# Kernel optimization log

Measured on AMD Instinct MI355X. Metric: run time of the kernel, lower is better.

## Reference

```python
import jax, jax.numpy as jnp
import numpy as np

B, NS, NT = 8, 1024, 1024
SRC, TGT, OUT, H = 1024, 1024, 1024, 8
DH = OUT // H  # per-head dim = 128


def setup_inputs() -> dict:
    key = jax.random.key(0)
    ks = jax.random.split(key, 9)
    s = 0.02
    return {
        "src": jax.random.normal(ks[0], (B, NS, SRC), jnp.float32),
        "tgt": jax.random.normal(ks[1], (B, NT, TGT), jnp.float32),
        "src_mask": jnp.ones((B, NS), jnp.float32),
        "tgt_mask": jnp.ones((B, NT), jnp.float32),
        "Ws": jax.random.normal(ks[2], (2 * OUT, SRC), jnp.float32) * s,
        "bs": jnp.zeros((2 * OUT,), jnp.float32),
        "Wt": jax.random.normal(ks[3], (OUT, TGT), jnp.float32) * s,
        "bt": jnp.zeros((OUT,), jnp.float32),
        "Wo": jax.random.normal(ks[4], (OUT, OUT + TGT), jnp.float32) * s,
        "bo": jnp.zeros((OUT,), jnp.float32),
    }


def reference(src, tgt, src_mask, tgt_mask, Ws, bs, Wt, bt, Wo, bo):
    # src_lin / tgt_lin (FCNet = linear, no activation, drop=0 at eval)
    src_trans = jnp.einsum("bsf,of->bso", src, Ws) + bs  # [B,NS,2*OUT]
    tgt_trans = jnp.einsum("btf,of->bto", tgt, Wt) + bt  # [B,NT,OUT]
    src_trans = src_trans * src_mask[:, :, None]
    tgt_trans = tgt_trans * tgt_mask[:, :, None]

    src_key, src_val = jnp.split(src_trans, 2, axis=2)  # each [B,NS,OUT]
    # head split along channels == reshape to [.., H, DH]
    k = src_key.reshape(B, NS, H, DH)
    v = src_val.reshape(B, NS, H, DH)
    q = tgt_trans.reshape(B, NT, H, DH)

    scores = jnp.einsum("bthd,bshd->bhts", q, k) / jnp.sqrt(jnp.float32(DH))
    scores = jnp.where(src_mask[:, None, None, :] == 0, -jnp.inf, scores)
    attn = jax.nn.softmax(scores, axis=-1)  # [B,H,NT,NS]
    tgt_update = jnp.einsum("bhts,bshd->bthd", attn, v).reshape(B, NT, OUT)

    cat_tgt = jnp.concatenate([tgt, tgt_update], axis=2)  # [B,NT,TGT+OUT]
    update_tgt = jnp.einsum("btf,of->bto", cat_tgt, Wo) + bo
    return update_tgt
```

## Files before the change

### kernel.cpp

```cpp
#include <hip/hip_runtime.h>


typedef __bf16 bf16x8 __attribute__((ext_vector_type(8)));
typedef float f32x4 __attribute__((ext_vector_type(4)));
typedef unsigned short u16;
typedef unsigned short u16x8 __attribute__((ext_vector_type(8)));

#define MFMA16(a, b, c) __builtin_amdgcn_mfma_f32_16x16x32_bf16((a), (b), (c), 0, 0, 0)

__device__ __forceinline__ float bf2f(u16 b) {
  return __uint_as_float(((unsigned)b) << 16);
}
__device__ __forceinline__ u16 f2bf(float f) {
  unsigned u = __float_as_uint(f);
  u += 0x7fffu + ((u >> 16) & 1u);
  return (u16)(u >> 16);
}

__device__ __forceinline__ void async16(const u16* g, u16* l) {
  __builtin_amdgcn_global_load_lds(
      (const __attribute__((address_space(1))) unsigned int*)g,
      (__attribute__((address_space(3))) unsigned int*)l, 16, 0, 0);
}

struct Cvt5 {
  const float* src[5];
  unsigned cnt4[5];
  unsigned ooff[5];
};

__global__ __launch_bounds__(256)
void cvt5_kernel(Cvt5 a, u16* __restrict__ out, unsigned total4)
{
  unsigned gid = blockIdx.x * 256u + threadIdx.x;
  if (gid >= total4) return;
  unsigned rem = gid;
  int s = 0;
  while (s < 4 && rem >= a.cnt4[s]) { rem -= a.cnt4[s]; ++s; }
  const float4 v = ((const float4*)a.src[s])[rem];
  ushort4 o;
  o.x = f2bf(v.x); o.y = f2bf(v.y); o.z = f2bf(v.z); o.w = f2bf(v.w);
  *(ushort4*)(out + a.ooff[s] + (size_t)rem * 4) = o;
}

template <int MODE, typename OutT>
__global__ __launch_bounds__(256, 2)
void gemm_bt_kernel(const u16* __restrict__ A0, const u16* __restrict__ A1,
                    int splitK,
                    const u16* __restrict__ Bw, const float* __restrict__ bias,
                    const float* __restrict__ rowscale,
                    OutT* __restrict__ C, int N, int K)
{
  __shared__ u16 As[128 * 32];
  __shared__ u16 Bs[128 * 32];
  const int tid  = threadIdx.x;
  const int lane = tid & 63;
  const int w    = tid >> 6;
  const int wm = w >> 1, wn = w & 1;
  const int quad = lane >> 4, lr = lane & 15;
  const unsigned nwg  = gridDim.x * gridDim.y;
  const unsigned wgid = blockIdx.y * gridDim.x + blockIdx.x;
  const unsigned swz  = (wgid & 7u) * (nwg >> 3) + (wgid >> 3);
  const int m0 = (int)(swz / gridDim.x) * 128;
  const int n0 = (int)(swz % gridDim.x) * 128;

  const f32x4 z4 = {0.f, 0.f, 0.f, 0.f};
  f32x4 acc[4][4];
#pragma unroll
  for (int i = 0; i < 4; ++i)
#pragma unroll
    for (int j = 0; j < 4; ++j)
      acc[i][j] = z4;

  const int acol = (tid & 3) * 8;

  for (int k0 = 0; k0 < K; k0 += 32) {
    const u16* Ap; int lda, kk;
    if (k0 < splitK) { Ap = A0; lda = splitK;     kk = k0; }
    else             { Ap = A1; lda = K - splitK; kk = k0 - splitK; }
    __syncthreads();
#pragma unroll
    for (int it = 0; it < 2; ++it) {
      const int row = it * 64 + (tid >> 2);
      const int ldsbase = (it * 256 + (tid & 192)) * 8;
      async16(Ap + (size_t)(m0 + row) * lda + (kk + acol), &As[ldsbase]);
      async16(Bw + (size_t)(n0 + row) * K   + (k0 + acol), &Bs[ldsbase]);
    }
    __syncthreads();

    bf16x8 af[4], bfr[4];
#pragma unroll
    for (int i = 0; i < 4; ++i)
      af[i] = *(const bf16x8*)&As[(wm * 64 + i * 16 + lr) * 32 + quad * 8];
#pragma unroll
    for (int j = 0; j < 4; ++j)
      bfr[j] = *(const bf16x8*)&Bs[(wn * 64 + j * 16 + lr) * 32 + quad * 8];
#pragma unroll
    for (int i = 0; i < 4; ++i)
#pragma unroll
      for (int j = 0; j < 4; ++j)
        acc[i][j] = MFMA16(af[i], bfr[j], acc[i][j]);
  }

  float bv[4];
#pragma unroll
  for (int j = 0; j < 4; ++j)
    bv[j] = bias[n0 + wn * 64 + j * 16 + lr];

#pragma unroll
  for (int i = 0; i < 4; ++i)
#pragma unroll
    for (int r = 0; r < 4; ++r) {
      const int grow = m0 + wm * 64 + i * 16 + quad * 4 + r;
      float rs = 1.f;
      if (rowscale) rs = rowscale[grow];
#pragma unroll
      for (int j = 0; j < 4; ++j) {
        const int gcol = n0 + wn * 64 + j * 16 + lr;
        const float val = (acc[i][j][r] + bv[j]) * rs;
        if (MODE == 0) {
          C[(size_t)grow * N + gcol] = (OutT)val;
        } else {
          const int b = grow >> 10, s = grow & 1023;
          size_t off;
          if (gcol < 1024) {
            const int h = gcol >> 7, d = gcol & 127;
            off = ((((size_t)(b * 8 + h) * 16 + (d >> 3)) * 1024 + s) * 8) + (d & 7);
          } else {
            const int cc = gcol - 1024;
            const int h = cc >> 7, d = cc & 127;
            off = (size_t)8388608 +
                  ((((size_t)(b * 8 + h) * 16 + (s >> 6)) * 1024 +
                    ((s >> 3) & 7) * 128 + d) * 8) + (s & 7);
          }
          ((u16*)C)[off] = f2bf(val);
        }
      }
    }
}

template <>
__global__ __launch_bounds__(256, 2)
void gemm_bt_kernel<0, u16>(const u16* __restrict__ A0, const u16* __restrict__ A1,
                            int splitK,
                            const u16* __restrict__ Bw, const float* __restrict__ bias,
                            const float* __restrict__ rowscale,
                            u16* __restrict__ C, int N, int K)
{
  __shared__ u16 As[128 * 32];
  __shared__ u16 Bs[128 * 32];
  const int tid  = threadIdx.x;
  const int lane = tid & 63;
  const int w    = tid >> 6;
  const int wm = w >> 1, wn = w & 1;
  const int quad = lane >> 4, lr = lane & 15;
  const unsigned nwg  = gridDim.x * gridDim.y;
  const unsigned wgid = blockIdx.y * gridDim.x + blockIdx.x;
  const unsigned swz  = (wgid & 7u) * (nwg >> 3) + (wgid >> 3);
  const int m0 = (int)(swz / gridDim.x) * 128;
  const int n0 = (int)(swz % gridDim.x) * 128;

  const f32x4 z4 = {0.f, 0.f, 0.f, 0.f};
  f32x4 acc[4][4];
#pragma unroll
  for (int i = 0; i < 4; ++i)
#pragma unroll
    for (int j = 0; j < 4; ++j)
      acc[i][j] = z4;

  const int acol = (tid & 3) * 8;

  for (int k0 = 0; k0 < K; k0 += 32) {
    const u16* Ap; int lda, kk;
    if (k0 < splitK) { Ap = A0; lda = splitK;     kk = k0; }
    else             { Ap = A1; lda = K - splitK; kk = k0 - splitK; }
    __syncthreads();
#pragma unroll
    for (int it = 0; it < 2; ++it) {
      const int row = it * 64 + (tid >> 2);
      const int ldsbase = (it * 256 + (tid & 192)) * 8;
      async16(Ap + (size_t)(m0 + row) * lda + (kk + acol), &As[ldsbase]);
      async16(Bw + (size_t)(n0 + row) * K   + (k0 + acol), &Bs[ldsbase]);
    }
    __syncthreads();

    bf16x8 af[4], bfr[4];
#pragma unroll
    for (int i = 0; i < 4; ++i)
      af[i] = *(const bf16x8*)&As[(wm * 64 + i * 16 + lr) * 32 + quad * 8];
#pragma unroll
    for (int j = 0; j < 4; ++j)
      bfr[j] = *(const bf16x8*)&Bs[(wn * 64 + j * 16 + lr) * 32 + quad * 8];
#pragma unroll
    for (int i = 0; i < 4; ++i)
#pragma unroll
      for (int j = 0; j < 4; ++j)
        acc[i][j] = MFMA16(af[i], bfr[j], acc[i][j]);
  }

  float bv[4];
#pragma unroll
  for (int j = 0; j < 4; ++j)
    bv[j] = bias[n0 + wn * 64 + j * 16 + lr];

#pragma unroll
  for (int i = 0; i < 4; ++i)
#pragma unroll
    for (int r = 0; r < 4; ++r) {
      const int grow = m0 + wm * 64 + i * 16 + quad * 4 + r;
      float rs = 1.f;
      if (rowscale) rs = rowscale[grow];
#pragma unroll
      for (int j = 0; j < 4; ++j) {
        const int gcol = n0 + wn * 64 + j * 16 + lr;
        C[(size_t)grow * N + gcol] = f2bf((acc[i][j][r] + bv[j]) * rs);
      }
    }
}

#define SCLOG2E 0.12751813754618667f

__global__ __launch_bounds__(256, 4)
void flash_kernel(const u16* __restrict__ q, const u16* __restrict__ Kg,
                  const u16* __restrict__ Vg,
                  const float* __restrict__ smask, u16* __restrict__ upd)
{
  __shared__ u16 Ks[64 * 128];
  __shared__ u16 Vs[64 * 128];
  __shared__ u16 Ps[4][16 * 64];

  const int tid  = threadIdx.x;
  const int lane = tid & 63;
  const int w    = tid >> 6;
  const int quad = lane >> 4, lr = lane & 15;
  const int bh_i = blockIdx.x;
  const int qt   = blockIdx.y;
  const int b = bh_i >> 3, h = bh_i & 7;
  const size_t bh = (size_t)bh_i;

  const size_t qrow0 = (size_t)b * 1024 + qt * 64 + w * 16;

  bf16x8 qf[4];
#pragma unroll
  for (int kk = 0; kk < 4; ++kk)
    qf[kk] = *(const bf16x8*)&q[(qrow0 + lr) * 1024 + h * 128 + kk * 32 + quad * 8];

  const f32x4 z4 = {0.f, 0.f, 0.f, 0.f};
  f32x4 oacc[8];
#pragma unroll
  for (int jd = 0; jd < 8; ++jd) oacc[jd] = z4;
  float lsum[4] = {0.f, 0.f, 0.f, 0.f};

  for (int s0 = 0; s0 < 1024; s0 += 64) {
    const int t = s0 >> 6;
    __syncthreads();
#pragma unroll
    for (int it = 0; it < 4; ++it) {
      const int dc = it * 4 + w;
      async16(Kg + (((bh * 16 + dc) * 1024) + s0 + lane) * 8,
              &Ks[(it * 256 + (tid & 192)) * 8]);
    }
#pragma unroll
    for (int it = 0; it < 4; ++it) {
      const int f = it * 256 + tid;
      async16(Vg + ((bh * 16 + t) * 1024 + f) * 8,
              &Vs[(it * 256 + (tid & 192)) * 8]);
    }
    __syncthreads();

    f32x4 sacc[4];
#pragma unroll
    for (int j = 0; j < 4; ++j) sacc[j] = z4;
    __builtin_amdgcn_s_setprio(1);
#pragma unroll
    for (int kk = 0; kk < 4; ++kk) {
      bf16x8 kb[4];
#pragma unroll
      for (int j = 0; j < 4; ++j)
        kb[j] = *(const bf16x8*)&Ks[((kk * 4 + quad) * 64 + j * 16 + lr) * 8];
#pragma unroll
      for (int j = 0; j < 4; ++j)
        sacc[j] = MFMA16(qf[kk], kb[j], sacc[j]);
    }
    __builtin_amdgcn_s_setprio(0);

    float mb[4];
#pragma unroll
    for (int j = 0; j < 4; ++j) {
      const float mv = smask[b * 1024 + s0 + j * 16 + lr];
      mb[j] = (mv == 0.f) ? -1e30f : 0.f;
    }

#pragma unroll
    for (int r = 0; r < 4; ++r) {
      const int row = quad * 4 + r;
      const int rsw = (row & 7) * 8;
      float ps = 0.f;
#pragma unroll
      for (int j = 0; j < 4; ++j) {
        const float p = exp2f(fmaf(sacc[j][r], SCLOG2E, mb[j]));
        ps += p;
        Ps[w][row * 64 + ((j * 16 + lr) ^ rsw)] = f2bf(p);
      }
      lsum[r] += ps;
    }

    __builtin_amdgcn_s_setprio(1);
#pragma unroll
    for (int kk2 = 0; kk2 < 2; ++kk2) {
      bf16x8 pa, vb[8];
      pa = *(const bf16x8*)&Ps[w][lr * 64 + ((kk2 * 32 + quad * 8) ^ ((lr & 7) * 8))];
#pragma unroll
      for (int jd = 0; jd < 8; ++jd)
        vb[jd] = *(const bf16x8*)&Vs[((kk2 * 4 + quad) * 128 + jd * 16 + lr) * 8];
#pragma unroll
      for (int jd = 0; jd < 8; ++jd)
        oacc[jd] = MFMA16(pa, vb[jd], oacc[jd]);
    }
    __builtin_amdgcn_s_setprio(0);
  }

#pragma unroll
  for (int r = 0; r < 4; ++r) {
    float l = lsum[r];
    l += __shfl_xor(l, 1);
    l += __shfl_xor(l, 2);
    l += __shfl_xor(l, 4);
    l += __shfl_xor(l, 8);
    const float inv = 1.f / l;
    const size_t grow = qrow0 + quad * 4 + r;
#pragma unroll
    for (int jd = 0; jd < 8; ++jd)
      upd[grow * 1024 + h * 128 + jd * 16 + lr] = f2bf(oacc[jd][r] * inv);
  }
}

__global__ void magic_kernel(float* out, float val)
{
  if (threadIdx.x == 0 && blockIdx.x == 0) out[0] = val;
}

extern "C" void kernel_launch(void* const* d_in, const int* in_sizes, int n_in,
                              void* d_out, int out_size, void* d_ws, size_t ws_size,
                              hipStream_t stream)
{
  static const int dict_sz[10]   = {8388608, 8388608, 8192, 8192, 2097152,
                                    2048, 1048576, 1024, 2097152, 1024};
  static const int sorted_sz[10] = {2097152, 2097152, 1048576, 1024, 2048,
                                    1024, 8388608, 8192, 8388608, 8192};
  bool is_dict = (n_in == 10), is_sorted = (n_in == 10);
  if (n_in == 10) {
    for (int i = 0; i < 10; ++i) {
      if (in_sizes[i] != dict_sz[i])   is_dict = false;
      if (in_sizes[i] != sorted_sz[i]) is_sorted = false;
    }
  }

  const float *src, *tgt, *smask, *tmask, *Ws, *bs, *Wt, *bt, *Wo, *bo;
  if (is_sorted) {
    Wo    = (const float*)d_in[0];
    Ws    = (const float*)d_in[1];
    Wt    = (const float*)d_in[2];
    bo    = (const float*)d_in[3];
    bs    = (const float*)d_in[4];
    bt    = (const float*)d_in[5];
    src   = (const float*)d_in[6];
    smask = (const float*)d_in[7];
    tgt   = (const float*)d_in[8];
    tmask = (const float*)d_in[9];
  } else {
    src   = (const float*)d_in[0];
    tgt   = (const float*)d_in[1];
    smask = (const float*)d_in[2];
    tmask = (const float*)d_in[3];
    Ws    = (const float*)d_in[4];
    bs    = (const float*)d_in[5];
    Wt    = (const float*)d_in[6];
    bt    = (const float*)d_in[7];
    Wo    = (const float*)d_in[8];
    bo    = (const float*)d_in[9];
  }
  float* out = (float*)d_out;

  const size_t KV = 16777216, Q = 8388608, UPD = 8388608;
  const unsigned segsz[5] = {8388608u, 8388608u, 2097152u, 1048576u, 2097152u};
  size_t total_u16 = KV + Q + UPD;
  unsigned aoff[5], off = 0, total4 = 0;
  for (int i = 0; i < 5; ++i) {
    aoff[i] = off;
    off += segsz[i];
    total4 += segsz[i] / 4u;
  }
  total_u16 += off;

  unsigned ws_mb = (unsigned)(ws_size >> 20);
  if (ws_mb > 999u) ws_mb = 999u;
  if (!is_dict && !is_sorted) {
    magic_kernel<<<dim3(1), dim3(64), 0, stream>>>(out, 4000.f + (float)ws_mb);
    return;
  }
  if (ws_size < total_u16 * 2) {
    magic_kernel<<<dim3(1), dim3(64), 0, stream>>>(out, 3000.f + (float)ws_mb);
    return;
  }

  u16* kvbuf  = (u16*)d_ws;
  u16* qbuf   = kvbuf + KV;
  u16* updbuf = qbuf + Q;
  u16* arena  = updbuf + UPD;

  Cvt5 ca;
  const float* segp[5] = {src, tgt, Ws, Wt, Wo};
  for (int i = 0; i < 5; ++i) {
    ca.src[i]  = segp[i];
    ca.cnt4[i] = segsz[i] / 4u;
    ca.ooff[i] = aoff[i];
  }
  const u16* srcb = arena + aoff[0];
  const u16* tgtb = arena + aoff[1];
  const u16* Wsb  = arena + aoff[2];
  const u16* Wtb  = arena + aoff[3];
  const u16* Wob  = arena + aoff[4];

  dim3 blk(256);
  cvt5_kernel<<<dim3((total4 + 255u) / 256u), blk, 0, stream>>>(ca, arena, total4);
  gemm_bt_kernel<1, u16><<<dim3(16, 64), blk, 0, stream>>>(
      srcb, nullptr, 1024, Wsb, bs, smask, kvbuf, 2048, 1024);
  gemm_bt_kernel<0, u16><<<dim3(8, 64), blk, 0, stream>>>(
      tgtb, nullptr, 1024, Wtb, bt, tmask, qbuf, 1024, 1024);
  flash_kernel<<<dim3(64, 16), blk, 0, stream>>>(
      qbuf, kvbuf, kvbuf + 8388608, smask, updbuf);
  gemm_bt_kernel<0, float><<<dim3(8, 64), blk, 0, stream>>>(
      tgtb, updbuf, 1024, Wob, bo, nullptr, out, 1024, 2048);
}
```

Baseline: 322.1 us.

## Double-buffer K/V tiles in flash kernel with async prefetch and mask lookahead

The flash attention kernel now keeps two LDS buffers for K and V. It prefetches the tile two steps ahead with async global-to-LDS loads, synchronising through a vmcnt wait and raw barriers, so memory latency overlaps the MFMA work. The mask values for the next tile are loaded one iteration early, and bf16 conversion switches to the hardware cast. The larger LDS footprint lowers the occupancy bound from 4 to 2 blocks, and the final iterations issue redundant wraparound prefetches.

```diff
diff --git a/kernel.cpp b/kernel.cpp
--- a/kernel.cpp
+++ b/kernel.cpp
@@ -15,6 +15,10 @@
   unsigned u = __float_as_uint(f);
   u += 0x7fffu + ((u >> 16) & 1u);
   return (u16)(u >> 16);
+}
+__device__ __forceinline__ u16 f2bf_hw(float f) {
+  __bf16 h = (__bf16)f;
+  return __builtin_bit_cast(u16, h);
 }
 
 __device__ __forceinline__ void async16(const u16* g, u16* l) {
@@ -220,13 +224,13 @@
 
 #define SCLOG2E 0.12751813754618667f
 
-__global__ __launch_bounds__(256, 4)
+__global__ __launch_bounds__(256, 2)
 void flash_kernel(const u16* __restrict__ q, const u16* __restrict__ Kg,
                   const u16* __restrict__ Vg,
                   const float* __restrict__ smask, u16* __restrict__ upd)
 {
-  __shared__ u16 Ks[64 * 128];
-  __shared__ u16 Vs[64 * 128];
+  __shared__ u16 Ks[2][64 * 128];
+  __shared__ u16 Vs[2][64 * 128];
   __shared__ u16 Ps[4][16 * 64];
 
   const int tid  = threadIdx.x;
@@ -245,28 +249,51 @@
   for (int kk = 0; kk < 4; ++kk)
     qf[kk] = *(const bf16x8*)&q[(qrow0 + lr) * 1024 + h * 128 + kk * 32 + quad * 8];
 
-  const f32x4 z4 = {0.f, 0.f, 0.f, 0.f};
-  f32x4 oacc[8];
-#pragma unroll
-  for (int jd = 0; jd < 8; ++jd) oacc[jd] = z4;
-  float lsum[4] = {0.f, 0.f, 0.f, 0.f};
-
-  for (int s0 = 0; s0 < 1024; s0 += 64) {
-    const int t = s0 >> 6;
-    __syncthreads();
+  float mvn[4];
+#pragma unroll
+  for (int j = 0; j < 4; ++j)
+    mvn[j] = smask[b * 1024 + j * 16 + lr];
+
+  auto stage = [&](int t, int bb) {
+    const int s0 = t * 64;
 #pragma unroll
     for (int it = 0; it < 4; ++it) {
       const int dc = it * 4 + w;
       async16(Kg + (((bh * 16 + dc) * 1024) + s0 + lane) * 8,
-              &Ks[(it * 256 + (tid & 192)) * 8]);
+              &Ks[bb][(it * 256 + (tid & 192)) * 8]);
     }
 #pragma unroll
     for (int it = 0; it < 4; ++it) {
-      const int f = it * 256 + tid;
-      async16(Vg + ((bh * 16 + t) * 1024 + f) * 8,
-              &Vs[(it * 256 + (tid & 192)) * 8]);
-    }
-    __syncthreads();
+      async16(Vg + ((bh * 16 + t) * 1024 + it * 256 + tid) * 8,
+              &Vs[bb][(it * 256 + (tid & 192)) * 8]);
+    }
+  };
+
+  const f32x4 z4 = {0.f, 0.f, 0.f, 0.f};
+  f32x4 oacc[8];
+#pragma unroll
+  for (int jd = 0; jd < 8; ++jd) oacc[jd] = z4;
+  float lsum[4] = {0.f, 0.f, 0.f, 0.f};
+
+  stage(0, 0);
+  stage(1, 1);
+
+#pragma unroll 1
+  for (int t = 0; t < 16; ++t) {
+    const int bb = t & 1;
+    asm volatile("s_waitcnt vmcnt(8)" ::: "memory");
+    __builtin_amdgcn_s_barrier();
+
+    float mb[4];
+#pragma unroll
+    for (int j = 0; j < 4; ++j)
+      mb[j] = (mvn[j] == 0.f) ? -1e30f : 0.f;
+    {
+      const int sn = ((t + 1) & 15) * 64;
+#pragma unroll
+      for (int j = 0; j < 4; ++j)
+        mvn[j] = smask[b * 1024 + sn + j * 16 + lr];
+    }
 
     f32x4 sacc[4];
 #pragma unroll
@@ -277,19 +304,12 @@
       bf16x8 kb[4];
 #pragma unroll
       for (int j = 0; j < 4; ++j)
-        kb[j] = *(const bf16x8*)&Ks[((kk * 4 + quad) * 64 + j * 16 + lr) * 8];
+        kb[j] = *(const bf16x8*)&Ks[bb][((kk * 4 + quad) * 64 + j * 16 + lr) * 8];
 #pragma unroll
       for (int j = 0; j < 4; ++j)
         sacc[j] = MFMA16(qf[kk], kb[j], sacc[j]);
     }
     __builtin_amdgcn_s_setprio(0);
-
-    float mb[4];
-#pragma unroll
-    for (int j = 0; j < 4; ++j) {
-      const float mv = smask[b * 1024 + s0 + j * 16 + lr];
-      mb[j] = (mv == 0.f) ? -1e30f : 0.f;
-    }
 
 #pragma unroll
     for (int r = 0; r < 4; ++r) {
@@ -300,7 +320,7 @@
       for (int j = 0; j < 4; ++j) {
         const float p = exp2f(fmaf(sacc[j][r], SCLOG2E, mb[j]));
         ps += p;
-        Ps[w][row * 64 + ((j * 16 + lr) ^ rsw)] = f2bf(p);
+        Ps[w][row * 64 + ((j * 16 + lr) ^ rsw)] = f2bf_hw(p);
       }
       lsum[r] += ps;
     }
@@ -312,13 +332,18 @@
       pa = *(const bf16x8*)&Ps[w][lr * 64 + ((kk2 * 32 + quad * 8) ^ ((lr & 7) * 8))];
 #pragma unroll
       for (int jd = 0; jd < 8; ++jd)
-        vb[jd] = *(const bf16x8*)&Vs[((kk2 * 4 + quad) * 128 + jd * 16 + lr) * 8];
+        vb[jd] = *(const bf16x8*)&Vs[bb][((kk2 * 4 + quad) * 128 + jd * 16 + lr) * 8];
 #pragma unroll
       for (int jd = 0; jd < 8; ++jd)
         oacc[jd] = MFMA16(pa, vb[jd], oacc[jd]);
     }
     __builtin_amdgcn_s_setprio(0);
-  }
+
+    __builtin_amdgcn_s_barrier();
+    stage((t + 2) & 15, bb);
+  }
+
+  asm volatile("s_waitcnt vmcnt(0)" ::: "memory");
 
 #pragma unroll
   for (int r = 0; r < 4; ++r) {
@@ -331,7 +356,7 @@
     const size_t grow = qrow0 + quad * 4 + r;
 #pragma unroll
     for (int jd = 0; jd < 8; ++jd)
-      upd[grow * 1024 + h * 128 + jd * 16 + lr] = f2bf(oacc[jd][r] * inv);
+      upd[grow * 1024 + h * 128 + jd * 16 + lr] = f2bf_hw(oacc[jd][r] * inv);
   }
 }
 
```

New measurement: 325.8 us. About the same (+1.2%).
